# Kernel optimization log

Measured on AMD Instinct MI355X. Metric: run time of the kernel, lower is better.

Reference implementation:

```python
import jax, jax.numpy as jnp
import numpy as np

N_LABELS = 24
LABEL_DIM = 256
NEG = -10000.0


def setup_inputs() -> dict:
    key = jax.random.key(0)
    k1, k2 = jax.random.split(key, 2)
    B, L, DIM = 8, 512, 1024
    features = jax.random.normal(k1, (B, L, DIM), dtype=jnp.float32)
    mask = jnp.ones((B, L), dtype=bool)
    w_ff = jax.random.normal(k2, (N_LABELS * LABEL_DIM * 2, DIM), dtype=jnp.float32) * 0.02
    b_ff = jnp.zeros((N_LABELS * LABEL_DIM * 2,), dtype=jnp.float32)
    bias = jnp.zeros((N_LABELS,), dtype=jnp.float32)
    return {"features": features, "mask": mask, "w_ff": w_ff, "b_ff": b_ff, "bias": bias}


def reference(features, mask, w_ff, b_ff, bias):
    B, L, _ = features.shape
    # ff -> relu -> split into start/end features per label
    x = jax.nn.relu(jnp.einsum('bld,od->blo', features, w_ff) + b_ff)  # [B,L,n_labels*label_dim*2]
    x = x.reshape(B, L, N_LABELS, LABEL_DIM, 2)
    start_f = x[..., 0]  # [B,L,n_labels,label_dim]
    end_f = x[..., 1]
    # biaffine pairwise span scores: [B, n_labels, start, end]
    scores = jnp.einsum('bsld,beld->blse', start_f, end_f) + bias[None, :, None, None]
    # remove_nan branch: replace inf/nan with -10000
    scores = jnp.where(jnp.isinf(scores) | jnp.isnan(scores), NEG, scores)
    # triangular + padding mask over (start, end)
    triu = jnp.triu(jnp.ones((L, L), dtype=bool))  # start <= end
    spans_mask = triu[None] & mask[:, :, None] & mask[:, None, :]  # [B,L,L]
    masked_scores = jnp.where(spans_mask[:, None, :, :], scores, NEG)
    return scores, masked_scores
```

## Files before the change

kernel.cpp:

```cpp
#include <hip/hip_runtime.h>
#include <hip/hip_bf16.h>

#define NLAB  24
#define LDIM  256
#define LSEQ  512
#define DDIM  1024
#define NOUT  12288
#define NEGV  (-10000.0f)
#define MOFF  50331648L

typedef __attribute__((ext_vector_type(8))) short short8;
typedef __attribute__((ext_vector_type(4))) float f32x4;
typedef unsigned short u16;
typedef unsigned int   u32;

typedef const __attribute__((address_space(1))) void gvoid_t;
typedef __attribute__((address_space(3))) void lvoid_t;

__device__ __forceinline__ u16 f2bf(float f) {
  u32 u = __builtin_bit_cast(u32, f);
  u32 r = u + 0x7FFFu + ((u >> 16) & 1u);
  return (u16)(r >> 16);
}

__device__ __forceinline__ void g2l16(const u16* g, u16* l) {
  __builtin_amdgcn_global_load_lds((gvoid_t*)g, (lvoid_t*)l, 16, 0, 0);
}

__global__ void cvt_bf16_kernel(const float* __restrict__ feat,
                                const float* __restrict__ wff,
                                u16* __restrict__ fA, u16* __restrict__ fB) {
  const long NA = 4194304L;
  const long NB = 12582912L;
  const long NQ = (NA + NB) / 4;
  long stride = (long)gridDim.x * blockDim.x;
  for (long i = (long)blockIdx.x * blockDim.x + threadIdx.x; i < NQ; i += stride) {
    long e = i * 4;
    const float* s; u16* d;
    if (e < NA) { s = feat + e;        d = fA + e; }
    else        { s = wff + (e - NA);  d = fB + (e - NA); }
    float4 v = *reinterpret_cast<const float4*>(s);
    ushort4 o;
    o.x = f2bf(v.x); o.y = f2bf(v.y); o.z = f2bf(v.z); o.w = f2bf(v.w);
    *reinterpret_cast<ushort4*>(d) = o;
  }
}

__global__ __launch_bounds__(512, 2)
void ff_gemm256(const u16* __restrict__ A, const u16* __restrict__ B,
                const float* __restrict__ bff,
                u16* __restrict__ sf, u16* __restrict__ ef) {
  __shared__ __align__(16) u16 lds[3][2][8192];
  const int tid = threadIdx.x, lane = tid & 63, wv = tid >> 6;
  const int wm = wv >> 2, wn = wv & 3;
  const int lr = lane & 15, hi = lane >> 4;

  const int bid = blockIdx.x;
  const int wg  = (bid & 7) * 96 + (bid >> 3);
  const int tm  = wg & 15, tn = wg >> 4;
  const int rowA0 = tm * 256, rowB0 = tn * 256;

  const u16* gAa[2]; const u16* gBa[2]; int dsta[2];
#pragma unroll
  for (int L = 0; L < 2; ++L) {
    const int g = L * 512 + tid;
    const int r = g >> 2;
    const int c = (g & 3) ^ ((g >> 3) & 3);
    gAa[L] = A + (long)(rowA0 + r) * DDIM + c * 8;
    const int gr = (r & ~31) | ((r & 15) << 1) | ((r >> 4) & 1);
    gBa[L] = B + (long)(rowB0 + gr) * DDIM + c * 8;
    dsta[L] = g * 8;
  }

  int offA[8], offB[4];
#pragma unroll
  for (int i = 0; i < 8; ++i) { const int r = wm * 128 + i * 16 + lr; offA[i] = (4 * r + (hi ^ ((r >> 1) & 3))) * 8; }
#pragma unroll
  for (int j = 0; j < 4; ++j) { const int r = wn * 64 + j * 16 + lr; offB[j] = (4 * r + (hi ^ ((r >> 1) & 3))) * 8; }

  f32x4 acc[8][4] = {};

#pragma unroll
  for (int L = 0; L < 2; ++L) g2l16(gAa[L],      &lds[0][0][dsta[L]]);
#pragma unroll
  for (int L = 0; L < 2; ++L) g2l16(gBa[L],      &lds[0][1][dsta[L]]);
#pragma unroll
  for (int L = 0; L < 2; ++L) g2l16(gAa[L] + 32, &lds[1][0][dsta[L]]);
#pragma unroll
  for (int L = 0; L < 2; ++L) g2l16(gBa[L] + 32, &lds[1][1][dsta[L]]);
  __builtin_amdgcn_sched_barrier(0);
  asm volatile("s_waitcnt vmcnt(4)" ::: "memory");
  __builtin_amdgcn_s_barrier();

  int slot = 0;
#pragma unroll 1
  for (int t = 0; t < 32; ++t) {
    const u16* La = lds[slot][0];
    const u16* Lb = lds[slot][1];
    short8 af[8], bfr[4];
#pragma unroll
    for (int i = 0; i < 8; ++i) af[i] = *reinterpret_cast<const short8*>(La + offA[i]);
#pragma unroll
    for (int j = 0; j < 4; ++j) bfr[j] = *reinterpret_cast<const short8*>(Lb + offB[j]);
    if (t < 30) {
      int ns = slot + 2; if (ns >= 3) ns -= 3;
      const int ko = (t + 2) * 32;
#pragma unroll
      for (int L = 0; L < 2; ++L) g2l16(gAa[L] + ko, &lds[ns][0][dsta[L]]);
#pragma unroll
      for (int L = 0; L < 2; ++L) g2l16(gBa[L] + ko, &lds[ns][1][dsta[L]]);
    }
    asm volatile("s_waitcnt lgkmcnt(0)" ::: "memory");
    __builtin_amdgcn_sched_barrier(0);
    __builtin_amdgcn_s_setprio(1);
#pragma unroll
    for (int i = 0; i < 8; ++i)
#pragma unroll
      for (int j = 0; j < 4; ++j)
        acc[i][j] = __builtin_amdgcn_mfma_f32_16x16x32_bf16(af[i], bfr[j], acc[i][j], 0, 0, 0);
    __builtin_amdgcn_s_setprio(0);
    __builtin_amdgcn_sched_barrier(0);
    if (t < 30)       asm volatile("s_waitcnt vmcnt(4)" ::: "memory");
    else if (t == 30) asm volatile("s_waitcnt vmcnt(0)" ::: "memory");
    __builtin_amdgcn_s_barrier();
    slot += 1; if (slot >= 3) slot -= 3;
  }

#pragma unroll
  for (int j = 0; j < 4; ++j) {
    const int cblk = wn * 64 + j * 16;
    const int o = rowB0 + (cblk & ~31) + 2 * lr + ((cblk >> 4) & 1);
    const float bv = bff[o];
    const int label = o >> 9, d = (o >> 1) & 255, se = o & 1;
    u16* dst = se ? ef : sf;
#pragma unroll
    for (int i = 0; i < 8; ++i) {
#pragma unroll
      for (int r = 0; r < 4; ++r) {
        const int m = rowA0 + wm * 128 + i * 16 + hi * 4 + r;
        const int b = m >> 9, ll = m & 511;
        float v = acc[i][j][r] + bv;
        v = v > 0.f ? v : 0.f;
        dst[((long)(b * NLAB + label) * LSEQ + ll) * LDIM + d] = f2bf(v);
      }
    }
  }
}

template<int LDK, bool PERM>
__device__ __forceinline__ void stage_tile(const u16* __restrict__ gbase, int row0,
                                           int k0, u16* lbuf, int t) {
#pragma unroll
  for (int l = 0; l < 4; ++l) {
    const int rt = l * 64 + (t >> 3);
    const int ce = ((t & 7) ^ (rt & 7)) << 3;
    int gr = rt;
    if (PERM) gr = (rt & ~31) | ((rt & 15) << 1) | ((rt >> 4) & 1);
    g2l16(gbase + (long)(row0 + gr) * LDK + k0 + ce, lbuf + (l * 512 + t) * 8);
  }
}

#define FRAG_OFF(r, ks, hi) (((r) * 64 + (ks) * 32 + (hi) * 8) ^ (((r) & 7) << 3))

__global__ __launch_bounds__(512, 2)
void biaffine256(const u16* __restrict__ sf, const u16* __restrict__ ef,
                 const float* __restrict__ bias, const int* __restrict__ mask,
                 float* __restrict__ out) {
  __shared__ __align__(16) u16 lds[2][2][16384];
  const int tid = threadIdx.x, lane = tid & 63, wv = tid >> 6;
  const int wm = wv >> 2, wn = wv & 3;
  const int lr = lane & 15, hi = lane >> 4;

  const int bid = blockIdx.x;
  const int wg  = (bid & 7) * 96 + (bid >> 3);
  const int bl  = wg >> 2, tile = wg & 3;
  const int tm  = tile >> 1, tn = tile & 1;
  const int b = bl / NLAB, label = bl - b * NLAB;
  const u16* Ab = sf + (long)bl * LSEQ * LDIM;
  const u16* Bb = ef + (long)bl * LSEQ * LDIM;
  const int rowA0 = tm * 256, rowB0 = tn * 256;

  f32x4 acc[8][4] = {};

  stage_tile<LDIM, false>(Ab, rowA0, 0, lds[0][0], tid);
  stage_tile<LDIM, false>(Bb, rowB0, 0, lds[0][1], tid);
  __syncthreads();

  int buf = 0;
  for (int t = 0; t < 4; ++t) {
    if (t < 3) {
      stage_tile<LDIM, false>(Ab, rowA0, (t + 1) * 64, lds[buf ^ 1][0], tid);
      stage_tile<LDIM, false>(Bb, rowB0, (t + 1) * 64, lds[buf ^ 1][1], tid);
    }
    const u16* La = lds[buf][0];
    const u16* Lb = lds[buf][1];
#pragma unroll
    for (int ks = 0; ks < 2; ++ks) {
      short8 af[8], bfr[4];
#pragma unroll
      for (int i = 0; i < 8; ++i) {
        const int r = wm * 128 + i * 16 + lr;
        af[i] = *reinterpret_cast<const short8*>(La + FRAG_OFF(r, ks, hi));
      }
#pragma unroll
      for (int j = 0; j < 4; ++j) {
        const int r = wn * 64 + j * 16 + lr;
        bfr[j] = *reinterpret_cast<const short8*>(Lb + FRAG_OFF(r, ks, hi));
      }
      __builtin_amdgcn_s_setprio(1);
#pragma unroll
      for (int i = 0; i < 8; ++i)
#pragma unroll
        for (int j = 0; j < 4; ++j)
          acc[i][j] = __builtin_amdgcn_mfma_f32_16x16x32_bf16(af[i], bfr[j], acc[i][j], 0, 0, 0);
      __builtin_amdgcn_s_setprio(0);
    }
    __syncthreads();
    buf ^= 1;
  }

  const float bv = bias[label];
  const long obase = (long)bl * LSEQ * LSEQ;
#pragma unroll
  for (int i = 0; i < 8; ++i) {
#pragma unroll
    for (int r = 0; r < 4; ++r) {
      const int s = rowA0 + wm * 128 + i * 16 + hi * 4 + r;
      const bool ms = (mask[b * LSEQ + s] != 0);
      const long rbase = obase + (long)s * LSEQ;
#pragma unroll
      for (int j = 0; j < 4; ++j) {
        const int e = rowB0 + wn * 64 + j * 16 + lr;
        float v = acc[i][j][r] + bv;
        u32 bits = __builtin_bit_cast(u32, v);
        if ((bits & 0x7F800000u) == 0x7F800000u) v = NEGV;
        out[rbase + e] = v;
        const bool keep = (s <= e) && ms && (mask[b * LSEQ + e] != 0);
        out[MOFF + rbase + e] = keep ? v : NEGV;
      }
    }
  }
}

extern "C" void kernel_launch(void* const* d_in, const int* in_sizes, int n_in,
                              void* d_out, int out_size, void* d_ws, size_t ws_size,
                              hipStream_t stream) {
  const float* feat = (const float*)d_in[0];
  const int*   mask = (const int*)d_in[1];
  const float* wff  = (const float*)d_in[2];
  const float* bff  = (const float*)d_in[3];
  const float* bias = (const float*)d_in[4];
  float* out = (float*)d_out;

  u16* fA = (u16*)d_ws;
  u16* fB = fA + 4194304L;
  u16* sf = fB + 12582912L;
  u16* ef = sf + 25165824L;

  cvt_bf16_kernel<<<2048, 256, 0, stream>>>(feat, wff, fA, fB);
  ff_gemm256<<<768, 512, 0, stream>>>(fA, fB, bff, sf, ef);
  biaffine256<<<768, 512, 0, stream>>>(sf, ef, bias, mask, out);
}
```

Measured before the change: 260.4 us.

## Shrink FF GEMM to 128x128 tiles, restage biaffine with K=32 steps and nontemporal stores

The FF GEMM moves from 256x256 tiles with a 3-stage async pipeline and 512 threads to 128x128 tiles, 256 threads, a simple double buffer and 3072 blocks. The biaffine kernel now stages K in 32-wide steps using the same swizzled layout as the GEMM, which halves LDS use. It also hoists the end-mask loads out of the inner loop and writes outputs with nontemporal stores. The smaller GEMM tiles give more blocks and occupancy at the cost of data reuse per tile, and dropping the explicit waitcnt pipelining may expose memory latency.

```diff
diff --git a/kernel.cpp b/kernel.cpp
--- a/kernel.cpp
+++ b/kernel.cpp
@@ -26,6 +26,8 @@
 __device__ __forceinline__ void g2l16(const u16* g, u16* l) {
   __builtin_amdgcn_global_load_lds((gvoid_t*)g, (lvoid_t*)l, 16, 0, 0);
 }
+
+#define RD_OFF(r, hi) ((4 * (r) + ((hi) ^ (((r) >> 1) & 3))) * 8)
 
 __global__ void cvt_bf16_kernel(const float* __restrict__ feat,
                                 const float* __restrict__ wff,
@@ -46,24 +48,24 @@
   }
 }
 
-__global__ __launch_bounds__(512, 2)
-void ff_gemm256(const u16* __restrict__ A, const u16* __restrict__ B,
+__global__ __launch_bounds__(256)
+void ff_gemm128(const u16* __restrict__ A, const u16* __restrict__ B,
                 const float* __restrict__ bff,
                 u16* __restrict__ sf, u16* __restrict__ ef) {
-  __shared__ __align__(16) u16 lds[3][2][8192];
+  __shared__ __align__(16) u16 lds[2][2][4096];
   const int tid = threadIdx.x, lane = tid & 63, wv = tid >> 6;
-  const int wm = wv >> 2, wn = wv & 3;
+  const int wm = wv >> 1, wn = wv & 1;
   const int lr = lane & 15, hi = lane >> 4;
 
   const int bid = blockIdx.x;
-  const int wg  = (bid & 7) * 96 + (bid >> 3);
-  const int tm  = wg & 15, tn = wg >> 4;
-  const int rowA0 = tm * 256, rowB0 = tn * 256;
+  const int wg  = (bid & 7) * 384 + (bid >> 3);
+  const int tm  = wg & 31, tn = wg >> 5;
+  const int rowA0 = tm * 128, rowB0 = tn * 128;
 
   const u16* gAa[2]; const u16* gBa[2]; int dsta[2];
 #pragma unroll
   for (int L = 0; L < 2; ++L) {
-    const int g = L * 512 + tid;
+    const int g = L * 256 + tid;
     const int r = g >> 2;
     const int c = (g & 3) ^ ((g >> 3) & 3);
     gAa[L] = A + (long)(rowA0 + r) * DDIM + c * 8;
@@ -72,58 +74,44 @@
     dsta[L] = g * 8;
   }
 
-  int offA[8], offB[4];
-#pragma unroll
-  for (int i = 0; i < 8; ++i) { const int r = wm * 128 + i * 16 + lr; offA[i] = (4 * r + (hi ^ ((r >> 1) & 3))) * 8; }
-#pragma unroll
-  for (int j = 0; j < 4; ++j) { const int r = wn * 64 + j * 16 + lr; offB[j] = (4 * r + (hi ^ ((r >> 1) & 3))) * 8; }
-
-  f32x4 acc[8][4] = {};
-
-#pragma unroll
-  for (int L = 0; L < 2; ++L) g2l16(gAa[L],      &lds[0][0][dsta[L]]);
-#pragma unroll
-  for (int L = 0; L < 2; ++L) g2l16(gBa[L],      &lds[0][1][dsta[L]]);
-#pragma unroll
-  for (int L = 0; L < 2; ++L) g2l16(gAa[L] + 32, &lds[1][0][dsta[L]]);
-#pragma unroll
-  for (int L = 0; L < 2; ++L) g2l16(gBa[L] + 32, &lds[1][1][dsta[L]]);
-  __builtin_amdgcn_sched_barrier(0);
-  asm volatile("s_waitcnt vmcnt(4)" ::: "memory");
-  __builtin_amdgcn_s_barrier();
-
-  int slot = 0;
+  int offA[4], offB[4];
+#pragma unroll
+  for (int i = 0; i < 4; ++i) { offA[i] = RD_OFF(wm * 64 + i * 16 + lr, hi); }
+#pragma unroll
+  for (int j = 0; j < 4; ++j) { offB[j] = RD_OFF(wn * 64 + j * 16 + lr, hi); }
+
+  f32x4 acc[4][4] = {};
+
+#pragma unroll
+  for (int L = 0; L < 2; ++L) g2l16(gAa[L], &lds[0][0][dsta[L]]);
+#pragma unroll
+  for (int L = 0; L < 2; ++L) g2l16(gBa[L], &lds[0][1][dsta[L]]);
+  __syncthreads();
+
 #pragma unroll 1
   for (int t = 0; t < 32; ++t) {
-    const u16* La = lds[slot][0];
-    const u16* Lb = lds[slot][1];
-    short8 af[8], bfr[4];
-#pragma unroll
-    for (int i = 0; i < 8; ++i) af[i] = *reinterpret_cast<const short8*>(La + offA[i]);
+    if (t < 31) {
+      const int ko = (t + 1) * 32, nb = (t + 1) & 1;
+#pragma unroll
+      for (int L = 0; L < 2; ++L) g2l16(gAa[L] + ko, &lds[nb][0][dsta[L]]);
+#pragma unroll
+      for (int L = 0; L < 2; ++L) g2l16(gBa[L] + ko, &lds[nb][1][dsta[L]]);
+    }
+    const u16* La = lds[t & 1][0];
+    const u16* Lb = lds[t & 1][1];
+    short8 af[4], bfr[4];
+#pragma unroll
+    for (int i = 0; i < 4; ++i) af[i] = *reinterpret_cast<const short8*>(La + offA[i]);
 #pragma unroll
     for (int j = 0; j < 4; ++j) bfr[j] = *reinterpret_cast<const short8*>(Lb + offB[j]);
-    if (t < 30) {
-      int ns = slot + 2; if (ns >= 3) ns -= 3;
-      const int ko = (t + 2) * 32;
-#pragma unroll
-      for (int L = 0; L < 2; ++L) g2l16(gAa[L] + ko, &lds[ns][0][dsta[L]]);
-#pragma unroll
-      for (int L = 0; L < 2; ++L) g2l16(gBa[L] + ko, &lds[ns][1][dsta[L]]);
-    }
-    asm volatile("s_waitcnt lgkmcnt(0)" ::: "memory");
-    __builtin_amdgcn_sched_barrier(0);
     __builtin_amdgcn_s_setprio(1);
 #pragma unroll
-    for (int i = 0; i < 8; ++i)
+    for (int i = 0; i < 4; ++i)
 #pragma unroll
       for (int j = 0; j < 4; ++j)
         acc[i][j] = __builtin_amdgcn_mfma_f32_16x16x32_bf16(af[i], bfr[j], acc[i][j], 0, 0, 0);
     __builtin_amdgcn_s_setprio(0);
-    __builtin_amdgcn_sched_barrier(0);
-    if (t < 30)       asm volatile("s_waitcnt vmcnt(4)" ::: "memory");
-    else if (t == 30) asm volatile("s_waitcnt vmcnt(0)" ::: "memory");
-    __builtin_amdgcn_s_barrier();
-    slot += 1; if (slot >= 3) slot -= 3;
+    __syncthreads();
   }
 
 #pragma unroll
@@ -134,10 +122,10 @@
     const int label = o >> 9, d = (o >> 1) & 255, se = o & 1;
     u16* dst = se ? ef : sf;
 #pragma unroll
-    for (int i = 0; i < 8; ++i) {
+    for (int i = 0; i < 4; ++i) {
 #pragma unroll
       for (int r = 0; r < 4; ++r) {
-        const int m = rowA0 + wm * 128 + i * 16 + hi * 4 + r;
+        const int m = rowA0 + wm * 64 + i * 16 + hi * 4 + r;
         const int b = m >> 9, ll = m & 511;
         float v = acc[i][j][r] + bv;
         v = v > 0.f ? v : 0.f;
@@ -147,26 +135,11 @@
   }
 }
 
-template<int LDK, bool PERM>
-__device__ __forceinline__ void stage_tile(const u16* __restrict__ gbase, int row0,
-                                           int k0, u16* lbuf, int t) {
-#pragma unroll
-  for (int l = 0; l < 4; ++l) {
-    const int rt = l * 64 + (t >> 3);
-    const int ce = ((t & 7) ^ (rt & 7)) << 3;
-    int gr = rt;
-    if (PERM) gr = (rt & ~31) | ((rt & 15) << 1) | ((rt >> 4) & 1);
-    g2l16(gbase + (long)(row0 + gr) * LDK + k0 + ce, lbuf + (l * 512 + t) * 8);
-  }
-}
-
-#define FRAG_OFF(r, ks, hi) (((r) * 64 + (ks) * 32 + (hi) * 8) ^ (((r) & 7) << 3))
-
-__global__ __launch_bounds__(512, 2)
+__global__ __launch_bounds__(512)
 void biaffine256(const u16* __restrict__ sf, const u16* __restrict__ ef,
                  const float* __restrict__ bias, const int* __restrict__ mask,
                  float* __restrict__ out) {
-  __shared__ __align__(16) u16 lds[2][2][16384];
+  __shared__ __align__(16) u16 lds[2][2][8192];
   const int tid = threadIdx.x, lane = tid & 63, wv = tid >> 6;
   const int wm = wv >> 2, wn = wv & 3;
   const int lr = lane & 15, hi = lane >> 4;
@@ -180,47 +153,62 @@
   const u16* Bb = ef + (long)bl * LSEQ * LDIM;
   const int rowA0 = tm * 256, rowB0 = tn * 256;
 
+  const u16* gAa[2]; const u16* gBa[2]; int dsta[2];
+#pragma unroll
+  for (int L = 0; L < 2; ++L) {
+    const int g = L * 512 + tid;
+    const int r = g >> 2;
+    const int c = (g & 3) ^ ((g >> 3) & 3);
+    gAa[L] = Ab + (long)(rowA0 + r) * LDIM + c * 8;
+    gBa[L] = Bb + (long)(rowB0 + r) * LDIM + c * 8;
+    dsta[L] = g * 8;
+  }
+
+  int offA[8], offB[4];
+#pragma unroll
+  for (int i = 0; i < 8; ++i) { offA[i] = RD_OFF(wm * 128 + i * 16 + lr, hi); }
+#pragma unroll
+  for (int j = 0; j < 4; ++j) { offB[j] = RD_OFF(wn * 64 + j * 16 + lr, hi); }
+
   f32x4 acc[8][4] = {};
 
-  stage_tile<LDIM, false>(Ab, rowA0, 0, lds[0][0], tid);
-  stage_tile<LDIM, false>(Bb, rowB0, 0, lds[0][1], tid);
+#pragma unroll
+  for (int L = 0; L < 2; ++L) g2l16(gAa[L], &lds[0][0][dsta[L]]);
+#pragma unroll
+  for (int L = 0; L < 2; ++L) g2l16(gBa[L], &lds[0][1][dsta[L]]);
   __syncthreads();
 
-  int buf = 0;
-  for (int t = 0; t < 4; ++t) {
-    if (t < 3) {
-      stage_tile<LDIM, false>(Ab, rowA0, (t + 1) * 64, lds[buf ^ 1][0], tid);
-      stage_tile<LDIM, false>(Bb, rowB0, (t + 1) * 64, lds[buf ^ 1][1], tid);
-    }
-    const u16* La = lds[buf][0];
-    const u16* Lb = lds[buf][1];
-#pragma unroll
-    for (int ks = 0; ks < 2; ++ks) {
-      short8 af[8], bfr[4];
-#pragma unroll
-      for (int i = 0; i < 8; ++i) {
-        const int r = wm * 128 + i * 16 + lr;
-        af[i] = *reinterpret_cast<const short8*>(La + FRAG_OFF(r, ks, hi));
-      }
-#pragma unroll
-      for (int j = 0; j < 4; ++j) {
-        const int r = wn * 64 + j * 16 + lr;
-        bfr[j] = *reinterpret_cast<const short8*>(Lb + FRAG_OFF(r, ks, hi));
-      }
-      __builtin_amdgcn_s_setprio(1);
-#pragma unroll
-      for (int i = 0; i < 8; ++i)
-#pragma unroll
-        for (int j = 0; j < 4; ++j)
-          acc[i][j] = __builtin_amdgcn_mfma_f32_16x16x32_bf16(af[i], bfr[j], acc[i][j], 0, 0, 0);
-      __builtin_amdgcn_s_setprio(0);
-    }
+#pragma unroll 1
+  for (int t = 0; t < 8; ++t) {
+    if (t < 7) {
+      const int ko = (t + 1) * 32, nb = (t + 1) & 1;
+#pragma unroll
+      for (int L = 0; L < 2; ++L) g2l16(gAa[L] + ko, &lds[nb][0][dsta[L]]);
+#pragma unroll
+      for (int L = 0; L < 2; ++L) g2l16(gBa[L] + ko, &lds[nb][1][dsta[L]]);
+    }
+    const u16* La = lds[t & 1][0];
+    const u16* Lb = lds[t & 1][1];
+    short8 af[8], bfr[4];
+#pragma unroll
+    for (int i = 0; i < 8; ++i) af[i] = *reinterpret_cast<const short8*>(La + offA[i]);
+#pragma unroll
+    for (int j = 0; j < 4; ++j) bfr[j] = *reinterpret_cast<const short8*>(Lb + offB[j]);
+    __builtin_amdgcn_s_setprio(1);
+#pragma unroll
+    for (int i = 0; i < 8; ++i)
+#pragma unroll
+      for (int j = 0; j < 4; ++j)
+        acc[i][j] = __builtin_amdgcn_mfma_f32_16x16x32_bf16(af[i], bfr[j], acc[i][j], 0, 0, 0);
+    __builtin_amdgcn_s_setprio(0);
     __syncthreads();
-    buf ^= 1;
   }
 
   const float bv = bias[label];
   const long obase = (long)bl * LSEQ * LSEQ;
+  bool me[4];
+#pragma unroll
+  for (int j = 0; j < 4; ++j) me[j] = (mask[b * LSEQ + rowB0 + wn * 64 + j * 16 + lr] != 0);
 #pragma unroll
   for (int i = 0; i < 8; ++i) {
 #pragma unroll
@@ -234,9 +222,9 @@
         float v = acc[i][j][r] + bv;
         u32 bits = __builtin_bit_cast(u32, v);
         if ((bits & 0x7F800000u) == 0x7F800000u) v = NEGV;
-        out[rbase + e] = v;
-        const bool keep = (s <= e) && ms && (mask[b * LSEQ + e] != 0);
-        out[MOFF + rbase + e] = keep ? v : NEGV;
+        __builtin_nontemporal_store(v, &out[rbase + e]);
+        const bool keep = (s <= e) && ms && me[j];
+        __builtin_nontemporal_store(keep ? v : NEGV, &out[MOFF + rbase + e]);
       }
     }
   }
@@ -258,6 +246,6 @@
   u16* ef = sf + 25165824L;
 
   cvt_bf16_kernel<<<2048, 256, 0, stream>>>(feat, wff, fA, fB);
-  ff_gemm256<<<768, 512, 0, stream>>>(fA, fB, bff, sf, ef);
+  ff_gemm128<<<3072, 256, 0, stream>>>(fA, fB, bff, sf, ef);
   biaffine256<<<768, 512, 0, stream>>>(sf, ef, bias, mask, out);
 }
```

Result: slower. 281.8 us (+8.2%).
